# Optimization experiments

Measured on AMD Instinct MI355X. Metric: run time of the kernel, lower is better.

Reference implementation:

```python
import jax, jax.numpy as jnp
import numpy as np

R0 = 1.0
N_NODES = 10000
N_EDGES = 160000
DIM_A, DIM_V, DIM_D, CHAN = 64, 32, 16, 16

# Levi-Civita tensor for the antisymmetric (cross-product-like) products
_EPS = np.zeros((3, 3, 3), dtype=np.float32)
for (i, j, k), s in (((0,1,2),1.),((1,2,0),1.),((2,0,1),1.),((0,2,1),-1.),((2,1,0),-1.),((1,0,2),-1.)):
    _EPS[i, j, k] = s


def _tl(W, x):
    """TensLinear: mix channel axis 1 of x (B, din, *(3,)*rank) with W (dout, din)."""
    y = jnp.tensordot(x, W, axes=((1,), (1,)))  # (B, *(3,)*rank, dout)
    return jnp.moveaxis(y, -1, 1)


def radial_encode_8(r, r0):
    # 8 Gaussian radial basis functions on |r|/r0
    d = jnp.linalg.norm(r, axis=-1)            # (E,)
    x = d * (8.0 / r0)
    mu = jnp.arange(8, dtype=r.dtype)
    return jnp.exp(-0.5 * (x[:, None] - mu[None, :]) ** 2)  # (E, 8)


def tens_sigmoid_1(v):
    # equivariant squashing: scale vector by tanh(|v|)/|v|
    n = jnp.linalg.norm(v, axis=-1, keepdims=True)
    return v * jnp.tanh(n) / (n + 1e-12)


def _forward(floats, src, dst, n_nodes):
    (r_ij, x_a, x_v, x_d, W_L0, W_L1, W_L2,
     W_Y000, W_Y110, W_Y220, W_Y011, W_Y101, W_Y121, W_Y211,
     W_Y022, W_Y202, W_Y112, W_Y222, W_Y111, W_Y212,
     W_enc, b_enc, W_dir, W1, b1, W2, b2, W3, b3) = floats
    eps = jnp.asarray(_EPS)
    rad = radial_encode_8(r_ij, R0) @ W_enc.T + b_enc        # (E, chan)
    r = tens_sigmoid_1(r_ij * (7.0 / R0))                    # (E, 3)
    phi_a = rad                                              # (E, chan)
    phi_v = rad[:, :, None] * r[:, None, :]                  # (E, chan, 3)
    phi_d = rad[:, :, None, None] * r[:, None, None, :] * r[:, None, :, None]  # (E, chan, 3, 3)
    # gather destination-node features per edge
    x_a_j = _tl(W_L0, x_a)[dst]                              # (E, chan)
    x_v_j = _tl(W_L1, x_v)[dst]                              # (E, chan, 3)
    x_d_j = _tl(W_L2, x_d)[dst]                              # (E, chan, 3, 3)
    # equivariant tensor products (Bee.apply)
    y_000 = x_a_j * phi_a
    y_110 = jnp.sum(x_v_j * phi_v, -1)
    y_220 = jnp.sum(x_d_j * phi_d, (-2, -1))
    y_011 = x_a_j[..., None] * phi_v
    y_101 = x_v_j * phi_a[..., None]
    y_121 = jnp.einsum('ecj,ecji->eci', x_v_j, phi_d)
    y_211 = jnp.einsum('ecij,ecj->eci', x_d_j, phi_v)
    y_022 = x_a_j[..., None, None] * phi_d
    y_202 = x_d_j * phi_a[..., None, None]
    y_112 = x_v_j[..., :, None] * phi_v[..., None, :]
    y_222 = jnp.einsum('ecik,eckj->ecij', x_d_j, phi_d)
    y_111 = jnp.cross(x_v_j, phi_v)
    y_212 = jnp.einsum('ikl,eckj,ecl->ecij', eps, x_d_j, phi_v)
    psi_a = _tl(W_Y000, y_000) + _tl(W_Y110, y_110) + _tl(W_Y220, y_220)
    psi_v = (_tl(W_Y011, y_011) + _tl(W_Y101, y_101) + _tl(W_Y121, y_121)
             + _tl(W_Y211, y_211) + _tl(W_Y111, y_111))
    psi_d = (_tl(W_Y022, y_022) + _tl(W_Y202, y_202) + _tl(W_Y112, y_112)
             + _tl(W_Y222, y_222) + _tl(W_Y212, y_212))
    # residual MLP on the scalar channel: lin_direct(x) + layers(x)
    lrelu = lambda x: jnp.where(x >= 0, x, 0.1 * x)
    h = lrelu(psi_a @ W1.T + b1)
    h = lrelu(h @ W2.T + b2)
    psi_a = psi_a + psi_a @ W_dir.T + (h @ W3.T + b3)
    # scatter-reduce messages to source nodes
    B_a = jax.ops.segment_sum(psi_a, src, num_segments=n_nodes)
    B_v = jax.ops.segment_sum(psi_v, src, num_segments=n_nodes)
    B_d = jax.ops.segment_sum(psi_d, src, num_segments=n_nodes)
    return 0.1 * B_a, 0.1 * B_v, 0.1 * B_d


def setup_inputs() -> dict:
    key = jax.random.key(0)
    ks = jax.random.split(key, 32)
    f32 = jnp.float32
    nrm = lambda k, shape, scale=1.0: scale * jax.random.normal(k, shape, dtype=f32)
    E, N = N_EDGES, N_NODES
    sC = CHAN ** -0.5
    inp = {
        'r_ij': nrm(ks[0], (E, 3)),
        'x_a': nrm(ks[1], (N, DIM_A)),
        'x_v': nrm(ks[2], (N, DIM_V, 3)),
        'x_d': nrm(ks[3], (N, DIM_D, 3, 3)),
        'W_L0': nrm(ks[4], (CHAN, DIM_A), DIM_A ** -0.5),
        'W_L1': nrm(ks[5], (CHAN, DIM_V), DIM_V ** -0.5),
        'W_L2': nrm(ks[6], (CHAN, DIM_D), DIM_D ** -0.5),
        'W_Y000': nrm(ks[7], (DIM_A, CHAN), sC),
        'W_Y110': nrm(ks[8], (DIM_A, CHAN), sC),
        'W_Y220': nrm(ks[9], (DIM_A, CHAN), sC),
        'W_Y011': nrm(ks[10], (DIM_V, CHAN), sC),
        'W_Y101': nrm(ks[11], (DIM_V, CHAN), sC),
        'W_Y121': nrm(ks[12], (DIM_V, CHAN), sC),
        'W_Y211': nrm(ks[13], (DIM_V, CHAN), sC),
        'W_Y022': nrm(ks[14], (DIM_D, CHAN), sC),
        'W_Y202': nrm(ks[15], (DIM_D, CHAN), sC),
        'W_Y112': nrm(ks[16], (DIM_D, CHAN), sC),
        'W_Y222': nrm(ks[17], (DIM_D, CHAN), sC),
        'W_Y111': nrm(ks[18], (DIM_V, CHAN), sC),
        'W_Y212': nrm(ks[19], (DIM_D, CHAN), sC),
        'W_enc': nrm(ks[20], (CHAN, 8), 8 ** -0.5),
        'b_enc': jnp.zeros((CHAN,), f32),
        'W_dir': nrm(ks[21], (DIM_A, DIM_A), DIM_A ** -0.5),
        'W1': nrm(ks[22], (2 * DIM_A, DIM_A), DIM_A ** -0.5),
        'b1': jnp.zeros((2 * DIM_A,), f32),
        'W2': nrm(ks[23], (2 * DIM_A, 2 * DIM_A), (2 * DIM_A) ** -0.5),
        'b2': jnp.zeros((2 * DIM_A,), f32),
        'W3': nrm(ks[24], (DIM_A, 2 * DIM_A), (2 * DIM_A) ** -0.5),
        'b3': jnp.zeros((DIM_A,), f32),
        'src': jax.random.randint(ks[25], (E,), 0, N, dtype=jnp.int32),
        'dst': jax.random.randint(ks[26], (E,), 0, N, dtype=jnp.int32),
        'n_nodes': N,
    }
    return inp


def reference(r_ij, x_a, x_v, x_d, W_L0, W_L1, W_L2, W_Y000, W_Y110, W_Y220,
              W_Y011, W_Y101, W_Y121, W_Y211, W_Y022, W_Y202, W_Y112, W_Y222,
              W_Y111, W_Y212, W_enc, b_enc, W_dir, W1, b1, W2, b2, W3, b3,
              src, dst, n_nodes):
    floats = (r_ij, x_a, x_v, x_d, W_L0, W_L1, W_L2, W_Y000, W_Y110, W_Y220,
              W_Y011, W_Y101, W_Y121, W_Y211, W_Y022, W_Y202, W_Y112, W_Y222,
              W_Y111, W_Y212, W_enc, b_enc, W_dir, W1, b1, W2, b2, W3, b3)
    return _forward(floats, src, dst, n_nodes)
```

## Files before the change

kernel.cpp:

```cpp
#include <hip/hip_runtime.h>
#include <hip/hip_bf16.h>

typedef __hip_bfloat16 bf16;
typedef __attribute__((ext_vector_type(8))) short bf16x8;
typedef __attribute__((ext_vector_type(4))) float f32x4;

__device__ __forceinline__ short f2bb(float x) {
    bf16 h = __float2bfloat16(x);
    return *reinterpret_cast<short*>(&h);
}
__device__ __forceinline__ float bb2f(short s) {
    bf16 h = *reinterpret_cast<bf16*>(&s);
    return __bfloat162float(h);
}

__global__ void zero_i32(int* p, int n) {
    int i = blockIdx.x * blockDim.x + threadIdx.x;
    int stride = gridDim.x * blockDim.x;
    for (; i < n; i += stride) p[i] = 0;
}

__global__ void prep_w(
    const float* __restrict__ W000, const float* __restrict__ W110, const float* __restrict__ W220,
    const float* __restrict__ W011, const float* __restrict__ W101, const float* __restrict__ W121,
    const float* __restrict__ W211, const float* __restrict__ W111,
    const float* __restrict__ W022, const float* __restrict__ W202, const float* __restrict__ W112,
    const float* __restrict__ W222, const float* __restrict__ W212,
    const float* __restrict__ W1, const float* __restrict__ W2, const float* __restrict__ W3,
    const float* __restrict__ Wdir, bf16* __restrict__ out) {
    int i = blockIdx.x * 256 + threadIdx.x;
    if (i >= 45568) return;
    float v = 0.f;
    if (i < 4096) {
        int o = i >> 6, k = i & 63;
        if (k < 48) {
            int t = k >> 4, c = k & 15;
            const float* W = (t == 0) ? W000 : (t == 1) ? W110 : W220;
            v = W[o * 16 + c];
        }
    } else if (i < 7168) {
        int r = i - 4096, ch = r / 96, k = r % 96;
        if (k < 80) {
            int t = k >> 4, c = k & 15;
            const float* W = (t == 0) ? W011 : (t == 1) ? W101 : (t == 2) ? W121 : (t == 3) ? W211 : W111;
            v = W[ch * 16 + c];
        }
    } else if (i < 8704) {
        int r = i - 7168, ch = r / 96, k = r % 96;
        if (k < 80) {
            int t = k >> 4, c = k & 15;
            const float* W = (t == 0) ? W022 : (t == 1) ? W202 : (t == 2) ? W112 : (t == 3) ? W222 : W212;
            v = W[ch * 16 + c];
        }
    } else if (i < 16896) v = W1[i - 8704];
    else if (i < 33280) v = W2[i - 16896];
    else if (i < 41472) v = W3[i - 33280];
    else v = Wdir[i - 41472];
    out[i] = __float2bfloat16(v);
}

__global__ __launch_bounds__(256) void node_proj4(
    const float* __restrict__ xa, const float* __restrict__ xv, const float* __restrict__ xd,
    const float* __restrict__ WL0, const float* __restrict__ WL1, const float* __restrict__ WL2,
    float* __restrict__ Pa, float* __restrict__ Pv, float* __restrict__ Pd, int N) {
    __shared__ float sxa[256], sxv[384], sxd[576];
    const int n0 = blockIdx.x * 4;
    const int tid = threadIdx.x;
    if (n0 + tid / 64 < N) sxa[tid] = xa[(size_t)n0 * 64 + tid];
    for (int i = tid; i < 384; i += 256) if (n0 + i / 96 < N)  sxv[i] = xv[(size_t)n0 * 96 + i];
    for (int i = tid; i < 576; i += 256) if (n0 + i / 144 < N) sxd[i] = xd[(size_t)n0 * 144 + i];
    __syncthreads();
    for (int o = tid; o < 832; o += 256) {
        int ln = o / 208, s = o % 208;
        int n = n0 + ln;
        if (n >= N) continue;
        if (s < 16) {
            float a = 0.f;
            const float* w = WL0 + s * 64;
            const float* x = sxa + ln * 64;
            for (int d = 0; d < 64; ++d) a += w[d] * x[d];
            Pa[(size_t)n * 16 + s] = a;
        } else if (s < 64) {
            int idx = s - 16, c = idx / 3, i = idx % 3;
            float a = 0.f;
            const float* w = WL1 + c * 32;
            const float* x = sxv + ln * 96;
            for (int d = 0; d < 32; ++d) a += w[d] * x[d * 3 + i];
            Pv[(size_t)n * 48 + idx] = a;
        } else {
            int idx = s - 64, c = idx / 9, ij = idx % 9;
            float a = 0.f;
            const float* w = WL2 + c * 16;
            const float* x = sxd + ln * 144;
            for (int d = 0; d < 16; ++d) a += w[d] * x[d * 9 + ij];
            Pd[(size_t)n * 144 + idx] = a;
        }
    }
}

__global__ void hist_src(const int* __restrict__ src, int* __restrict__ cnt, int E) {
    int i = blockIdx.x * 256 + threadIdx.x;
    if (i < E) atomicAdd(&cnt[src[i]], 1);
}

__global__ void scan_rows(const int* __restrict__ cnt, int* __restrict__ rowstart, int N) {
    __shared__ int ps[256];
    int t = threadIdx.x;
    int chunk = (N + 255) / 256;
    int base = t * chunk;
    int s = 0;
    for (int i = 0; i < chunk; ++i) { int idx = base + i; if (idx < N) s += cnt[idx]; }
    ps[t] = s;
    __syncthreads();
    for (int off = 1; off < 256; off <<= 1) {
        int v = (t >= off) ? ps[t - off] : 0;
        __syncthreads();
        ps[t] += v;
        __syncthreads();
    }
    int run = (t > 0) ? ps[t - 1] : 0;
    for (int i = 0; i < chunk; ++i) {
        int idx = base + i;
        if (idx < N) { rowstart[idx] = run; run += cnt[idx]; }
    }
    if (t == 255) rowstart[N] = run;
}

__global__ void fill_slot(const int* __restrict__ src, const int* __restrict__ rowstart,
                          int* __restrict__ cursor, int* __restrict__ slot, int E) {
    int i = blockIdx.x * 256 + threadIdx.x;
    if (i < E) slot[i] = rowstart[src[i]] + atomicAdd(&cursor[src[i]], 1);
}

__global__ __launch_bounds__(256) void edge_mfma(
    const float* __restrict__ r_ij,
    const float* __restrict__ Pa, const float* __restrict__ Pv, const float* __restrict__ Pd,
    const float* __restrict__ Wenc, const float* __restrict__ benc,
    const bf16* __restrict__ Wa, const bf16* __restrict__ Wv, const bf16* __restrict__ Wd,
    const bf16* __restrict__ Wb1, const bf16* __restrict__ Wb2,
    const bf16* __restrict__ Wb3, const bf16* __restrict__ Wbdir,
    const float* __restrict__ b1, const float* __restrict__ b2, const float* __restrict__ b3,
    const int* __restrict__ slot, const int* __restrict__ dst,
    short* __restrict__ psi, int E)
{
    __shared__ __align__(16) char smem[32320];
    short* SYA   = (short*)smem;
    short* SYV   = (short*)(smem + 1536);
    short* SYD   = (short*)(smem + 9216);
    int*   SSLOT = (int*)(smem + 32256);
    short* SPSIA = (short*)(smem + 1536);
    short* SH1   = (short*)(smem + 3840);
    short* SH2   = (short*)(smem + 8192);
    short* SPSI  = (short*)(smem + 12544);

    const int tid = threadIdx.x;
    const int e0 = blockIdx.x * 16;
    const bf16x8 z8 = {};

    {
        const int le = tid >> 4, c = tid & 15;
        const int e = e0 + le;
        if (e < E) {
            const int j = dst[e];
            if (c == 0) SSLOT[le] = slot[e];
            float vx = 7.f * r_ij[e * 3 + 0];
            float vy = 7.f * r_ij[e * 3 + 1];
            float vz = 7.f * r_ij[e * 3 + 2];
            float nn = sqrtf(vx * vx + vy * vy + vz * vz);
            float sc = tanhf(nn) / (nn + 1e-12f);
            float rr[3] = {vx * sc, vy * sc, vz * sc};
            float x8 = nn * (8.f / 7.f);
            float rad = benc[c];
            #pragma unroll
            for (int m = 0; m < 8; ++m) {
                float tt = x8 - (float)m;
                rad += __expf(-0.5f * tt * tt) * Wenc[c * 8 + m];
            }
            float xa = Pa[j * 16 + c];
            float xv[3], xd[9];
            #pragma unroll
            for (int i = 0; i < 3; ++i) xv[i] = Pv[j * 48 + c * 3 + i];
            #pragma unroll
            for (int k = 0; k < 9; ++k) xd[k] = Pd[j * 144 + c * 9 + k];
            float dotv = xv[0] * rr[0] + xv[1] * rr[1] + xv[2] * rr[2];
            float mv[3];
            #pragma unroll
            for (int i = 0; i < 3; ++i)
                mv[i] = xd[i * 3] * rr[0] + xd[i * 3 + 1] * rr[1] + xd[i * 3 + 2] * rr[2];
            float quad = mv[0] * rr[0] + mv[1] * rr[1] + mv[2] * rr[2];
            SYA[le * 48 + c]      = f2bb(xa * rad);
            SYA[le * 48 + 16 + c] = f2bb(rad * dotv);
            SYA[le * 48 + 32 + c] = f2bb(rad * quad);
            #pragma unroll
            for (int i = 0; i < 3; ++i) {
                int row = (le * 3 + i) * 80;
                int i1 = (i + 1) % 3, i2 = (i + 2) % 3;
                SYV[row + c]      = f2bb(xa * rad * rr[i]);
                SYV[row + 16 + c] = f2bb(rad * xv[i]);
                SYV[row + 32 + c] = f2bb(rad * dotv * rr[i]);
                SYV[row + 48 + c] = f2bb(rad * mv[i]);
                SYV[row + 64 + c] = f2bb(rad * (xv[i1] * rr[i2] - xv[i2] * rr[i1]));
            }
            #pragma unroll
            for (int i = 0; i < 3; ++i) {
                int i1 = (i + 1) % 3, i2 = (i + 2) % 3;
                #pragma unroll
                for (int jj = 0; jj < 3; ++jj) {
                    int row = (le * 9 + i * 3 + jj) * 80;
                    SYD[row + c]      = f2bb(xa * rad * rr[i] * rr[jj]);
                    SYD[row + 16 + c] = f2bb(rad * xd[i * 3 + jj]);
                    SYD[row + 32 + c] = f2bb(rad * xv[i] * rr[jj]);
                    SYD[row + 48 + c] = f2bb(rad * mv[i] * rr[jj]);
                    SYD[row + 64 + c] = f2bb(rad * (xd[i1 * 3 + jj] * rr[i2] - xd[i2 * 3 + jj] * rr[i1]));
                }
            }
        }
    }
    __syncthreads();

    const int wid = tid >> 6, lane = tid & 63;
    const int q = lane >> 4, r16 = lane & 15;

    f32x4 da[4] = {};
    f32x4 dv[3][2] = {};
    f32x4 dd[5] = {};
    const int mstart = (wid == 2) ? 0 : 5;
    const int mcnt = (wid == 2) ? 5 : 4;

    if (wid == 0) {
        bf16x8 af0 = *(const bf16x8*)&SYA[r16 * 48 + q * 8];
        bf16x8 af1 = z8;
        if (q < 2) af1 = *(const bf16x8*)&SYA[r16 * 48 + 32 + q * 8];
        #pragma unroll
        for (int n = 0; n < 4; ++n) {
            bf16x8 bf0 = *(const bf16x8*)((const short*)Wa + (n * 16 + r16) * 64 + q * 8);
            bf16x8 bf1 = *(const bf16x8*)((const short*)Wa + (n * 16 + r16) * 64 + 32 + q * 8);
            da[n] = __builtin_amdgcn_mfma_f32_16x16x32_bf16(af0, bf0, da[n], 0, 0, 0);
            da[n] = __builtin_amdgcn_mfma_f32_16x16x32_bf16(af1, bf1, da[n], 0, 0, 0);
        }
    } else if (wid == 1) {
        #pragma unroll
        for (int ks = 0; ks < 3; ++ks) {
            bf16x8 av[3], bv[2];
            #pragma unroll
            for (int m = 0; m < 3; ++m) {
                if (ks < 2) av[m] = *(const bf16x8*)&SYV[(m * 16 + r16) * 80 + ks * 32 + q * 8];
                else {
                    av[m] = z8;
                    if (q < 2) av[m] = *(const bf16x8*)&SYV[(m * 16 + r16) * 80 + 64 + q * 8];
                }
            }
            #pragma unroll
            for (int n = 0; n < 2; ++n)
                bv[n] = *(const bf16x8*)((const short*)Wv + (n * 16 + r16) * 96 + ks * 32 + q * 8);
            #pragma unroll
            for (int m = 0; m < 3; ++m)
                #pragma unroll
                for (int n = 0; n < 2; ++n)
                    dv[m][n] = __builtin_amdgcn_mfma_f32_16x16x32_bf16(av[m], bv[n], dv[m][n], 0, 0, 0);
        }
    } else {
        #pragma unroll
        for (int ks = 0; ks < 3; ++ks) {
            bf16x8 bf = *(const bf16x8*)((const short*)Wd + r16 * 96 + ks * 32 + q * 8);
            for (int mi = 0; mi < mcnt; ++mi) {
                bf16x8 af;
                if (ks < 2) af = *(const bf16x8*)&SYD[((mstart + mi) * 16 + r16) * 80 + ks * 32 + q * 8];
                else {
                    af = z8;
                    if (q < 2) af = *(const bf16x8*)&SYD[((mstart + mi) * 16 + r16) * 80 + 64 + q * 8];
                }
                dd[mi] = __builtin_amdgcn_mfma_f32_16x16x32_bf16(af, bf, dd[mi], 0, 0, 0);
            }
        }
    }
    __syncthreads();

    if (wid == 0) {
        #pragma unroll
        for (int n = 0; n < 4; ++n)
            #pragma unroll
            for (int jj = 0; jj < 4; ++jj)
                SPSIA[(q * 4 + jj) * 72 + n * 16 + r16] = f2bb(da[n][jj]);
    } else if (wid == 1) {
        #pragma unroll
        for (int m = 0; m < 3; ++m)
            #pragma unroll
            for (int n = 0; n < 2; ++n)
                #pragma unroll
                for (int jj = 0; jj < 4; ++jj) {
                    int row = m * 16 + q * 4 + jj;
                    int el = row / 3, i = row % 3;
                    SPSI[el * 304 + 64 + (n * 16 + r16) * 3 + i] = f2bb(dv[m][n][jj]);
                }
    } else {
        for (int mi = 0; mi < mcnt; ++mi)
            #pragma unroll
            for (int jj = 0; jj < 4; ++jj) {
                int row = (mstart + mi) * 16 + q * 4 + jj;
                int el = row / 9, ij = row % 9;
                SPSI[el * 304 + 160 + r16 * 9 + ij] = f2bb(dd[mi][jj]);
            }
    }
    __syncthreads();

    {
        f32x4 h1a[2] = {};
        #pragma unroll
        for (int ks = 0; ks < 2; ++ks) {
            bf16x8 af = *(const bf16x8*)&SPSIA[r16 * 72 + ks * 32 + q * 8];
            #pragma unroll
            for (int n = 0; n < 2; ++n) {
                int col = wid * 32 + n * 16 + r16;
                bf16x8 bf = *(const bf16x8*)((const short*)Wb1 + col * 64 + ks * 32 + q * 8);
                h1a[n] = __builtin_amdgcn_mfma_f32_16x16x32_bf16(af, bf, h1a[n], 0, 0, 0);
            }
        }
        #pragma unroll
        for (int n = 0; n < 2; ++n) {
            int col = wid * 32 + n * 16 + r16;
            float bias = b1[col];
            #pragma unroll
            for (int jj = 0; jj < 4; ++jj) {
                float v = h1a[n][jj] + bias;
                v = v >= 0.f ? v : 0.1f * v;
                SH1[(q * 4 + jj) * 136 + col] = f2bb(v);
            }
        }
    }
    __syncthreads();
    {
        f32x4 h2a[2] = {};
        #pragma unroll
        for (int ks = 0; ks < 4; ++ks) {
            bf16x8 af = *(const bf16x8*)&SH1[r16 * 136 + ks * 32 + q * 8];
            #pragma unroll
            for (int n = 0; n < 2; ++n) {
                int col = wid * 32 + n * 16 + r16;
                bf16x8 bf = *(const bf16x8*)((const short*)Wb2 + col * 128 + ks * 32 + q * 8);
                h2a[n] = __builtin_amdgcn_mfma_f32_16x16x32_bf16(af, bf, h2a[n], 0, 0, 0);
            }
        }
        #pragma unroll
        for (int n = 0; n < 2; ++n) {
            int col = wid * 32 + n * 16 + r16;
            float bias = b2[col];
            #pragma unroll
            for (int jj = 0; jj < 4; ++jj) {
                float v = h2a[n][jj] + bias;
                v = v >= 0.f ? v : 0.1f * v;
                SH2[(q * 4 + jj) * 136 + col] = f2bb(v);
            }
        }
    }
    __syncthreads();
    {
        f32x4 o3 = {};
        const int col3 = wid * 16 + r16;
        #pragma unroll
        for (int ks = 0; ks < 4; ++ks) {
            bf16x8 af = *(const bf16x8*)&SH2[r16 * 136 + ks * 32 + q * 8];
            bf16x8 bf = *(const bf16x8*)((const short*)Wb3 + col3 * 128 + ks * 32 + q * 8);
            o3 = __builtin_amdgcn_mfma_f32_16x16x32_bf16(af, bf, o3, 0, 0, 0);
        }
        #pragma unroll
        for (int ks = 0; ks < 2; ++ks) {
            bf16x8 af = *(const bf16x8*)&SPSIA[r16 * 72 + ks * 32 + q * 8];
            bf16x8 bf = *(const bf16x8*)((const short*)Wbdir + col3 * 64 + ks * 32 + q * 8);
            o3 = __builtin_amdgcn_mfma_f32_16x16x32_bf16(af, bf, o3, 0, 0, 0);
        }
        float bias = b3[col3];
        #pragma unroll
        for (int jj = 0; jj < 4; ++jj) {
            int row = q * 4 + jj;
            float v = o3[jj] + bias + bb2f(SPSIA[row * 72 + col3]);
            SPSI[row * 304 + col3] = f2bb(v);
        }
    }
    __syncthreads();

    {
        const uint32_t* S32 = (const uint32_t*)SPSI;
        uint32_t* P32 = (uint32_t*)psi;
        for (int idx = tid; idx < 16 * 152; idx += 256) {
            int le = idx / 152, k = idx - le * 152;
            if (e0 + le < E)
                P32[(size_t)SSLOT[le] * 152 + k] = S32[le * 152 + k];
        }
    }
}

__global__ __launch_bounds__(192) void gather(
    const short* __restrict__ psi, const int* __restrict__ rowstart,
    float* __restrict__ out, int N) {
    int n = blockIdx.x, t = threadIdx.x;
    if (t >= 152) return;
    int s0 = rowstart[n], s1 = rowstart[n + 1];
    const uint32_t* p32 = (const uint32_t*)psi;
    float a0 = 0.f, a1 = 0.f;
    for (int s = s0; s < s1; ++s) {
        uint32_t u = p32[(size_t)s * 152 + t];
        a0 += __uint_as_float(u << 16);
        a1 += __uint_as_float(u & 0xffff0000u);
    }
    int f = 2 * t;
    float2 v = make_float2(0.1f * a0, 0.1f * a1);
    if (f < 64)       *(float2*)&out[(size_t)n * 64 + f] = v;
    else if (f < 160) *(float2*)&out[(size_t)N * 64 + (size_t)n * 96 + (f - 64)] = v;
    else              *(float2*)&out[(size_t)N * 160 + (size_t)n * 144 + (f - 160)] = v;
}

extern "C" void kernel_launch(void* const* d_in, const int* in_sizes, int n_in,
                              void* d_out, int out_size, void* d_ws, size_t ws_size,
                              hipStream_t stream) {
    const float* r_ij = (const float*)d_in[0];
    const float* x_a  = (const float*)d_in[1];
    const float* x_v  = (const float*)d_in[2];
    const float* x_d  = (const float*)d_in[3];
    const float* W_L0 = (const float*)d_in[4];
    const float* W_L1 = (const float*)d_in[5];
    const float* W_L2 = (const float*)d_in[6];
    const float* W000 = (const float*)d_in[7];
    const float* W110 = (const float*)d_in[8];
    const float* W220 = (const float*)d_in[9];
    const float* W011 = (const float*)d_in[10];
    const float* W101 = (const float*)d_in[11];
    const float* W121 = (const float*)d_in[12];
    const float* W211 = (const float*)d_in[13];
    const float* W022 = (const float*)d_in[14];
    const float* W202 = (const float*)d_in[15];
    const float* W112 = (const float*)d_in[16];
    const float* W222 = (const float*)d_in[17];
    const float* W111 = (const float*)d_in[18];
    const float* W212 = (const float*)d_in[19];
    const float* Wenc = (const float*)d_in[20];
    const float* benc = (const float*)d_in[21];
    const float* Wdir = (const float*)d_in[22];
    const float* W1   = (const float*)d_in[23];
    const float* b1   = (const float*)d_in[24];
    const float* W2   = (const float*)d_in[25];
    const float* b2   = (const float*)d_in[26];
    const float* W3   = (const float*)d_in[27];
    const float* b3   = (const float*)d_in[28];
    const int* src    = (const int*)d_in[29];
    const int* dst    = (const int*)d_in[30];

    const int E = in_sizes[29];
    const int N = in_sizes[1] / 64;

    float* Pa     = (float*)d_ws;
    float* Pv     = Pa + (size_t)N * 16;
    float* Pd     = Pv + (size_t)N * 48;
    bf16*  Wb     = (bf16*)(Pd + (size_t)N * 144);
    int*   cnt    = (int*)(Wb + 45568);
    int*   cursor = cnt + N;
    int*   rowst  = cursor + N;
    int*   slot   = rowst + N + 1;
    short* psi    = (short*)(slot + E);

    const bf16* Wa_p    = Wb;
    const bf16* Wv_p    = Wb + 4096;
    const bf16* Wd_p    = Wb + 7168;
    const bf16* Wb1_p   = Wb + 8704;
    const bf16* Wb2_p   = Wb + 16896;
    const bf16* Wb3_p   = Wb + 33280;
    const bf16* Wbdir_p = Wb + 41472;

    zero_i32<<<80, 256, 0, stream>>>(cnt, 2 * N);
    prep_w<<<178, 256, 0, stream>>>(W000, W110, W220, W011, W101, W121, W211, W111,
                                    W022, W202, W112, W222, W212, W1, W2, W3, Wdir, Wb);
    node_proj4<<<(N + 3) / 4, 256, 0, stream>>>(x_a, x_v, x_d, W_L0, W_L1, W_L2,
                                                Pa, Pv, Pd, N);
    hist_src<<<(E + 255) / 256, 256, 0, stream>>>(src, cnt, E);
    scan_rows<<<1, 256, 0, stream>>>(cnt, rowst, N);
    fill_slot<<<(E + 255) / 256, 256, 0, stream>>>(src, rowst, cursor, slot, E);
    edge_mfma<<<(E + 15) / 16, 256, 0, stream>>>(
        r_ij, Pa, Pv, Pd, Wenc, benc,
        Wa_p, Wv_p, Wd_p, Wb1_p, Wb2_p, Wb3_p, Wbdir_p,
        b1, b2, b3, slot, dst, psi, E);
    gather<<<N, 192, 0, stream>>>(psi, rowst, (float*)d_out, N);
}
```

Before: 245.1 us.

## Merge prep kernels, pad node projections for vector loads, use cheap bf16/tanh

Three setup kernels (weight conversion, node projection, source histogram) are merged into one launch by partitioning the grid across block ranges. The per-node projected vector and tensor features are padded to 4 and 12 floats per channel so the edge kernel can gather them with 16-byte vector loads. The float-to-bf16 conversion becomes a bit-trick round that does not handle NaN correctly and rounds ties away from zero rather than to even. tanhf is replaced with an exp plus hardware reciprocal formulation. These changes trade a little accuracy and a larger workspace for fewer launches and cheaper per-edge instructions.

```diff
diff --git a/kernel.cpp b/kernel.cpp
--- a/kernel.cpp
+++ b/kernel.cpp
@@ -5,13 +5,13 @@
 typedef __attribute__((ext_vector_type(8))) short bf16x8;
 typedef __attribute__((ext_vector_type(4))) float f32x4;
 
-__device__ __forceinline__ short f2bb(float x) {
-    bf16 h = __float2bfloat16(x);
-    return *reinterpret_cast<short*>(&h);
+__device__ __forceinline__ void st_bf16(short* p, float v) {
+    uint32_t u = __float_as_uint(v) + 0x8000u;
+    *p = (short)(u >> 16);
 }
 __device__ __forceinline__ float bb2f(short s) {
-    bf16 h = *reinterpret_cast<bf16*>(&s);
-    return __bfloat162float(h);
+    uint32_t u = ((uint32_t)(uint16_t)s) << 16;
+    return __uint_as_float(u);
 }
 
 __global__ void zero_i32(int* p, int n) {
@@ -20,86 +20,91 @@
     for (; i < n; i += stride) p[i] = 0;
 }
 
-__global__ void prep_w(
+__global__ __launch_bounds__(256) void prep_all(
     const float* __restrict__ W000, const float* __restrict__ W110, const float* __restrict__ W220,
     const float* __restrict__ W011, const float* __restrict__ W101, const float* __restrict__ W121,
     const float* __restrict__ W211, const float* __restrict__ W111,
     const float* __restrict__ W022, const float* __restrict__ W202, const float* __restrict__ W112,
     const float* __restrict__ W222, const float* __restrict__ W212,
     const float* __restrict__ W1, const float* __restrict__ W2, const float* __restrict__ W3,
-    const float* __restrict__ Wdir, bf16* __restrict__ out) {
-    int i = blockIdx.x * 256 + threadIdx.x;
-    if (i >= 45568) return;
-    float v = 0.f;
-    if (i < 4096) {
-        int o = i >> 6, k = i & 63;
-        if (k < 48) {
-            int t = k >> 4, c = k & 15;
-            const float* W = (t == 0) ? W000 : (t == 1) ? W110 : W220;
-            v = W[o * 16 + c];
-        }
-    } else if (i < 7168) {
-        int r = i - 4096, ch = r / 96, k = r % 96;
-        if (k < 80) {
-            int t = k >> 4, c = k & 15;
-            const float* W = (t == 0) ? W011 : (t == 1) ? W101 : (t == 2) ? W121 : (t == 3) ? W211 : W111;
-            v = W[ch * 16 + c];
-        }
-    } else if (i < 8704) {
-        int r = i - 7168, ch = r / 96, k = r % 96;
-        if (k < 80) {
-            int t = k >> 4, c = k & 15;
-            const float* W = (t == 0) ? W022 : (t == 1) ? W202 : (t == 2) ? W112 : (t == 3) ? W222 : W212;
-            v = W[ch * 16 + c];
-        }
-    } else if (i < 16896) v = W1[i - 8704];
-    else if (i < 33280) v = W2[i - 16896];
-    else if (i < 41472) v = W3[i - 33280];
-    else v = Wdir[i - 41472];
-    out[i] = __float2bfloat16(v);
-}
-
-__global__ __launch_bounds__(256) void node_proj4(
+    const float* __restrict__ Wdir, bf16* __restrict__ wout,
     const float* __restrict__ xa, const float* __restrict__ xv, const float* __restrict__ xd,
     const float* __restrict__ WL0, const float* __restrict__ WL1, const float* __restrict__ WL2,
-    float* __restrict__ Pa, float* __restrict__ Pv, float* __restrict__ Pd, int N) {
-    __shared__ float sxa[256], sxv[384], sxd[576];
-    const int n0 = blockIdx.x * 4;
+    float* __restrict__ Pa, float* __restrict__ Pv, float* __restrict__ Pd, int N, int NPB,
+    const int* __restrict__ src, int* __restrict__ cnt, int E)
+{
+    int b = blockIdx.x;
     const int tid = threadIdx.x;
-    if (n0 + tid / 64 < N) sxa[tid] = xa[(size_t)n0 * 64 + tid];
-    for (int i = tid; i < 384; i += 256) if (n0 + i / 96 < N)  sxv[i] = xv[(size_t)n0 * 96 + i];
-    for (int i = tid; i < 576; i += 256) if (n0 + i / 144 < N) sxd[i] = xd[(size_t)n0 * 144 + i];
-    __syncthreads();
-    for (int o = tid; o < 832; o += 256) {
-        int ln = o / 208, s = o % 208;
-        int n = n0 + ln;
-        if (n >= N) continue;
-        if (s < 16) {
-            float a = 0.f;
-            const float* w = WL0 + s * 64;
-            const float* x = sxa + ln * 64;
-            for (int d = 0; d < 64; ++d) a += w[d] * x[d];
-            Pa[(size_t)n * 16 + s] = a;
-        } else if (s < 64) {
-            int idx = s - 16, c = idx / 3, i = idx % 3;
-            float a = 0.f;
-            const float* w = WL1 + c * 32;
-            const float* x = sxv + ln * 96;
-            for (int d = 0; d < 32; ++d) a += w[d] * x[d * 3 + i];
-            Pv[(size_t)n * 48 + idx] = a;
-        } else {
-            int idx = s - 64, c = idx / 9, ij = idx % 9;
-            float a = 0.f;
-            const float* w = WL2 + c * 16;
-            const float* x = sxd + ln * 144;
-            for (int d = 0; d < 16; ++d) a += w[d] * x[d * 9 + ij];
-            Pd[(size_t)n * 144 + idx] = a;
-        }
-    }
-}
-
-__global__ void hist_src(const int* __restrict__ src, int* __restrict__ cnt, int E) {
-    int i = blockIdx.x * 256 + threadIdx.x;
+    if (b < 178) {
+        int i = b * 256 + tid;
+        if (i >= 45568) return;
+        float v = 0.f;
+        if (i < 4096) {
+            int o = i >> 6, k = i & 63;
+            if (k < 48) {
+                int t = k >> 4, c = k & 15;
+                const float* W = (t == 0) ? W000 : (t == 1) ? W110 : W220;
+                v = W[o * 16 + c];
+            }
+        } else if (i < 7168) {
+            int r = i - 4096, ch = r / 96, k = r % 96;
+            if (k < 80) {
+                int t = k >> 4, c = k & 15;
+                const float* W = (t == 0) ? W011 : (t == 1) ? W101 : (t == 2) ? W121 : (t == 3) ? W211 : W111;
+                v = W[ch * 16 + c];
+            }
+        } else if (i < 8704) {
+            int r = i - 7168, ch = r / 96, k = r % 96;
+            if (k < 80) {
+                int t = k >> 4, c = k & 15;
+                const float* W = (t == 0) ? W022 : (t == 1) ? W202 : (t == 2) ? W112 : (t == 3) ? W222 : W212;
+                v = W[ch * 16 + c];
+            }
+        } else if (i < 16896) v = W1[i - 8704];
+        else if (i < 33280) v = W2[i - 16896];
+        else if (i < 41472) v = W3[i - 33280];
+        else v = Wdir[i - 41472];
+        wout[i] = __float2bfloat16(v);
+        return;
+    }
+    b -= 178;
+    if (b < NPB) {
+        __shared__ float sxa[256], sxv[384], sxd[576];
+        const int n0 = b * 4;
+        if (n0 + tid / 64 < N) sxa[tid] = xa[(size_t)n0 * 64 + tid];
+        for (int i = tid; i < 384; i += 256) if (n0 + i / 96 < N)  sxv[i] = xv[(size_t)n0 * 96 + i];
+        for (int i = tid; i < 576; i += 256) if (n0 + i / 144 < N) sxd[i] = xd[(size_t)n0 * 144 + i];
+        __syncthreads();
+        for (int o = tid; o < 832; o += 256) {
+            int ln = o / 208, s = o % 208;
+            int n = n0 + ln;
+            if (n >= N) continue;
+            if (s < 16) {
+                float a = 0.f;
+                const float* w = WL0 + s * 64;
+                const float* x = sxa + ln * 64;
+                for (int d = 0; d < 64; ++d) a += w[d] * x[d];
+                Pa[(size_t)n * 16 + s] = a;
+            } else if (s < 64) {
+                int idx = s - 16, c = idx / 3, i = idx % 3;
+                float a = 0.f;
+                const float* w = WL1 + c * 32;
+                const float* x = sxv + ln * 96;
+                for (int d = 0; d < 32; ++d) a += w[d] * x[d * 3 + i];
+                Pv[(size_t)n * 64 + c * 4 + i] = a;
+            } else {
+                int idx = s - 64, c = idx / 9, ij = idx % 9;
+                float a = 0.f;
+                const float* w = WL2 + c * 16;
+                const float* x = sxd + ln * 144;
+                for (int d = 0; d < 16; ++d) a += w[d] * x[d * 9 + ij];
+                Pd[(size_t)n * 192 + c * 12 + ij] = a;
+            }
+        }
+        return;
+    }
+    b -= NPB;
+    int i = b * 256 + tid;
     if (i < E) atomicAdd(&cnt[src[i]], 1);
 }
 
@@ -167,7 +172,9 @@
             float vy = 7.f * r_ij[e * 3 + 1];
             float vz = 7.f * r_ij[e * 3 + 2];
             float nn = sqrtf(vx * vx + vy * vy + vz * vz);
-            float sc = tanhf(nn) / (nn + 1e-12f);
+            float ex = __expf(-2.f * nn);
+            float th = (1.f - ex) * __builtin_amdgcn_rcpf(1.f + ex);
+            float sc = th * __builtin_amdgcn_rcpf(nn + 1e-12f);
             float rr[3] = {vx * sc, vy * sc, vz * sc};
             float x8 = nn * (8.f / 7.f);
             float rad = benc[c];
@@ -177,29 +184,30 @@
                 rad += __expf(-0.5f * tt * tt) * Wenc[c * 8 + m];
             }
             float xa = Pa[j * 16 + c];
-            float xv[3], xd[9];
-            #pragma unroll
-            for (int i = 0; i < 3; ++i) xv[i] = Pv[j * 48 + c * 3 + i];
-            #pragma unroll
-            for (int k = 0; k < 9; ++k) xd[k] = Pd[j * 144 + c * 9 + k];
+            f32x4 pv4 = *(const f32x4*)(Pv + (size_t)j * 64 + c * 4);
+            f32x4 pd0 = *(const f32x4*)(Pd + (size_t)j * 192 + c * 12);
+            f32x4 pd1 = *(const f32x4*)(Pd + (size_t)j * 192 + c * 12 + 4);
+            f32x4 pd2 = *(const f32x4*)(Pd + (size_t)j * 192 + c * 12 + 8);
+            float xv[3] = {pv4[0], pv4[1], pv4[2]};
+            float xd[9] = {pd0[0], pd0[1], pd0[2], pd0[3], pd1[0], pd1[1], pd1[2], pd1[3], pd2[0]};
             float dotv = xv[0] * rr[0] + xv[1] * rr[1] + xv[2] * rr[2];
             float mv[3];
             #pragma unroll
             for (int i = 0; i < 3; ++i)
                 mv[i] = xd[i * 3] * rr[0] + xd[i * 3 + 1] * rr[1] + xd[i * 3 + 2] * rr[2];
             float quad = mv[0] * rr[0] + mv[1] * rr[1] + mv[2] * rr[2];
-            SYA[le * 48 + c]      = f2bb(xa * rad);
-            SYA[le * 48 + 16 + c] = f2bb(rad * dotv);
-            SYA[le * 48 + 32 + c] = f2bb(rad * quad);
+            st_bf16(&SYA[le * 48 + c],      xa * rad);
+            st_bf16(&SYA[le * 48 + 16 + c], rad * dotv);
+            st_bf16(&SYA[le * 48 + 32 + c], rad * quad);
             #pragma unroll
             for (int i = 0; i < 3; ++i) {
                 int row = (le * 3 + i) * 80;
                 int i1 = (i + 1) % 3, i2 = (i + 2) % 3;
-                SYV[row + c]      = f2bb(xa * rad * rr[i]);
-                SYV[row + 16 + c] = f2bb(rad * xv[i]);
-                SYV[row + 32 + c] = f2bb(rad * dotv * rr[i]);
-                SYV[row + 48 + c] = f2bb(rad * mv[i]);
-                SYV[row + 64 + c] = f2bb(rad * (xv[i1] * rr[i2] - xv[i2] * rr[i1]));
+                st_bf16(&SYV[row + c],      xa * rad * rr[i]);
+                st_bf16(&SYV[row + 16 + c], rad * xv[i]);
+                st_bf16(&SYV[row + 32 + c], rad * dotv * rr[i]);
+                st_bf16(&SYV[row + 48 + c], rad * mv[i]);
+                st_bf16(&SYV[row + 64 + c], rad * (xv[i1] * rr[i2] - xv[i2] * rr[i1]));
             }
             #pragma unroll
             for (int i = 0; i < 3; ++i) {
@@ -207,11 +215,11 @@
                 #pragma unroll
                 for (int jj = 0; jj < 3; ++jj) {
                     int row = (le * 9 + i * 3 + jj) * 80;
-                    SYD[row + c]      = f2bb(xa * rad * rr[i] * rr[jj]);
-                    SYD[row + 16 + c] = f2bb(rad * xd[i * 3 + jj]);
-                    SYD[row + 32 + c] = f2bb(rad * xv[i] * rr[jj]);
-                    SYD[row + 48 + c] = f2bb(rad * mv[i] * rr[jj]);
-                    SYD[row + 64 + c] = f2bb(rad * (xd[i1 * 3 + jj] * rr[i2] - xd[i2 * 3 + jj] * rr[i1]));
+                    st_bf16(&SYD[row + c],      xa * rad * rr[i] * rr[jj]);
+                    st_bf16(&SYD[row + 16 + c], rad * xd[i * 3 + jj]);
+                    st_bf16(&SYD[row + 32 + c], rad * xv[i] * rr[jj]);
+                    st_bf16(&SYD[row + 48 + c], rad * mv[i] * rr[jj]);
+                    st_bf16(&SYD[row + 64 + c], rad * (xd[i1 * 3 + jj] * rr[i2] - xd[i2 * 3 + jj] * rr[i1]));
                 }
             }
         }
@@ -281,7 +289,7 @@
         for (int n = 0; n < 4; ++n)
             #pragma unroll
             for (int jj = 0; jj < 4; ++jj)
-                SPSIA[(q * 4 + jj) * 72 + n * 16 + r16] = f2bb(da[n][jj]);
+                st_bf16(&SPSIA[(q * 4 + jj) * 72 + n * 16 + r16], da[n][jj]);
     } else if (wid == 1) {
         #pragma unroll
         for (int m = 0; m < 3; ++m)
@@ -291,7 +299,7 @@
                 for (int jj = 0; jj < 4; ++jj) {
                     int row = m * 16 + q * 4 + jj;
                     int el = row / 3, i = row % 3;
-                    SPSI[el * 304 + 64 + (n * 16 + r16) * 3 + i] = f2bb(dv[m][n][jj]);
+                    st_bf16(&SPSI[el * 304 + 64 + (n * 16 + r16) * 3 + i], dv[m][n][jj]);
                 }
     } else {
         for (int mi = 0; mi < mcnt; ++mi)
@@ -299,7 +307,7 @@
             for (int jj = 0; jj < 4; ++jj) {
                 int row = (mstart + mi) * 16 + q * 4 + jj;
                 int el = row / 9, ij = row % 9;
-                SPSI[el * 304 + 160 + r16 * 9 + ij] = f2bb(dd[mi][jj]);
+                st_bf16(&SPSI[el * 304 + 160 + r16 * 9 + ij], dd[mi][jj]);
             }
     }
     __syncthreads();
@@ -324,7 +332,7 @@
             for (int jj = 0; jj < 4; ++jj) {
                 float v = h1a[n][jj] + bias;
                 v = v >= 0.f ? v : 0.1f * v;
-                SH1[(q * 4 + jj) * 136 + col] = f2bb(v);
+                st_bf16(&SH1[(q * 4 + jj) * 136 + col], v);
             }
         }
     }
@@ -349,7 +357,7 @@
             for (int jj = 0; jj < 4; ++jj) {
                 float v = h2a[n][jj] + bias;
                 v = v >= 0.f ? v : 0.1f * v;
-                SH2[(q * 4 + jj) * 136 + col] = f2bb(v);
+                st_bf16(&SH2[(q * 4 + jj) * 136 + col], v);
             }
         }
     }
@@ -374,7 +382,7 @@
         for (int jj = 0; jj < 4; ++jj) {
             int row = q * 4 + jj;
             float v = o3[jj] + bias + bb2f(SPSIA[row * 72 + col3]);
-            SPSI[row * 304 + col3] = f2bb(v);
+            st_bf16(&SPSI[row * 304 + col3], v);
         }
     }
     __syncthreads();
@@ -450,8 +458,8 @@
 
     float* Pa     = (float*)d_ws;
     float* Pv     = Pa + (size_t)N * 16;
-    float* Pd     = Pv + (size_t)N * 48;
-    bf16*  Wb     = (bf16*)(Pd + (size_t)N * 144);
+    float* Pd     = Pv + (size_t)N * 64;
+    bf16*  Wb     = (bf16*)(Pd + (size_t)N * 192);
     int*   cnt    = (int*)(Wb + 45568);
     int*   cursor = cnt + N;
     int*   rowst  = cursor + N;
@@ -466,14 +474,17 @@
     const bf16* Wb3_p   = Wb + 33280;
     const bf16* Wbdir_p = Wb + 41472;
 
+    const int NPB = (N + 3) / 4;
+    const int HB  = (E + 255) / 256;
+
     zero_i32<<<80, 256, 0, stream>>>(cnt, 2 * N);
-    prep_w<<<178, 256, 0, stream>>>(W000, W110, W220, W011, W101, W121, W211, W111,
-                                    W022, W202, W112, W222, W212, W1, W2, W3, Wdir, Wb);
-    node_proj4<<<(N + 3) / 4, 256, 0, stream>>>(x_a, x_v, x_d, W_L0, W_L1, W_L2,
-                                                Pa, Pv, Pd, N);
-    hist_src<<<(E + 255) / 256, 256, 0, stream>>>(src, cnt, E);
+    prep_all<<<178 + NPB + HB, 256, 0, stream>>>(
+        W000, W110, W220, W011, W101, W121, W211, W111,
+        W022, W202, W112, W222, W212, W1, W2, W3, Wdir, Wb,
+        x_a, x_v, x_d, W_L0, W_L1, W_L2, Pa, Pv, Pd, N, NPB,
+        src, cnt, E);
     scan_rows<<<1, 256, 0, stream>>>(cnt, rowst, N);
-    fill_slot<<<(E + 255) / 256, 256, 0, stream>>>(src, rowst, cursor, slot, E);
+    fill_slot<<<HB, 256, 0, stream>>>(src, rowst, cursor, slot, E);
     edge_mfma<<<(E + 15) / 16, 256, 0, stream>>>(
         r_ij, Pa, Pv, Pd, Wenc, benc,
         Wa_p, Wv_p, Wd_p, Wb1_p, Wb2_p, Wb3_p, Wbdir_p,
```

After: 242.1 us. Within noise of the previous version (-1.2%).
